# Performance work log

Hardware: AMD Instinct MI355X
Metric: run time of the kernel (lower is better)

## Reference

```python
import jax, jax.numpy as jnp
import numpy as np

SIZE = 48          # grid edge
DIST = 4           # local neighborhood edge
PAD = DIST // 2    # padding = 2
PADDED = SIZE + 2 * PAD  # 52
RATE = 5           # recurrent steps
CONVEY = 0.9
N_IN = 2048        # input injection sites


def setup_inputs() -> dict:
    key = jax.random.key(0)
    ks = jax.random.split(key, 8)
    neuron_matrix = jnp.zeros((PADDED, PADDED, PADDED), dtype=jnp.float32)
    vinput = jax.random.normal(ks[0], (N_IN,), dtype=jnp.float32)
    # scale synapse so the 5-step relu recurrence stays numerically tame
    synapse = jax.random.normal(ks[1], (SIZE, SIZE, SIZE, DIST, DIST, DIST), dtype=jnp.float32) * 0.05
    W1 = jax.random.normal(ks[2], (SIZE ** 3, 1024), dtype=jnp.float32) * (1.0 / np.sqrt(SIZE ** 3))
    b1 = jnp.zeros((1024,), dtype=jnp.float32)
    W2 = jax.random.normal(ks[3], (1024, 128), dtype=jnp.float32) * (1.0 / np.sqrt(1024))
    b2 = jnp.zeros((128,), dtype=jnp.float32)
    W3 = jax.random.normal(ks[4], (128, 10), dtype=jnp.float32) * (1.0 / np.sqrt(128))
    b3 = jnp.zeros((10,), dtype=jnp.float32)
    node_idx = jax.random.randint(ks[5], (N_IN, 3), 0, SIZE)  # interior coords
    return {"neuron_matrix": neuron_matrix, "vinput": vinput, "synapse": synapse,
            "W1": W1, "b1": b1, "W2": W2, "b2": b2, "W3": W3, "b3": b3,
            "node_idx": node_idx}


def _windows(p):
    # p: [PADDED]^3 -> sliding DxDxD windows at every interior site: [S,S,S,D,D,D]
    idx = jnp.arange(SIZE)[:, None] + jnp.arange(DIST)[None, :]  # [S, D]
    w = jnp.take(p, idx, axis=0)   # [S, D, P, P]
    w = jnp.take(w, idx, axis=2)   # [S, D, S, D, P]
    w = jnp.take(w, idx, axis=4)   # [S, D, S, D, S, D]
    return jnp.transpose(w, (0, 2, 4, 1, 3, 5))  # [S, S, S, D, D, D]


def reference(neuron_matrix, vinput, synapse, W1, b1, W2, b2, W3, b3, node_idx):
    # inject inputs at (possibly colliding) interior nodes (scatter-add, like +=)
    nm = neuron_matrix.at[node_idx[:, 0] + PAD,
                          node_idx[:, 1] + PAD,
                          node_idx[:, 2] + PAD].add(vinput)
    # recurrent locally-connected 3D neighbor aggregation, RATE steps
    for _ in range(RATE):
        win = _windows(nm)  # [S,S,S,D,D,D]
        agg = jnp.einsum('xyzabc,xyzabc->xyz', synapse, win)  # per-site unique-weight reduce
        interior = jax.nn.relu(agg) * CONVEY
        nm = jnp.pad(interior, PAD)  # re-pad with zeros for next step
    x = interior.reshape(1, SIZE ** 3)
    x = jax.nn.relu(x @ W1 + b1)
    x = jax.nn.relu(x @ W2 + b2)
    return x @ W3 + b3  # [1, 10]
```

## Files before the change

kernel.cpp:

```cpp
#include <hip/hip_runtime.h>

#define S 48
#define D 4
#define PADC 2
#define P 52
#define SITES (S * S * S)
#define PADVOL (P * P * P)
#define N_IN 2048
#define H1 1024
#define H2 128
#define OUTN 10
#define RP 64
#define NCH (SITES / RP)
#define RG 16
#define CHPG (NCH / RG)
#define G2B 32

__global__ __launch_bounds__(256) void zero_k(float4* __restrict__ p, int n4) {
    int i = blockIdx.x * 256 + threadIdx.x;
    if (i < n4) p[i] = make_float4(0.f, 0.f, 0.f, 0.f);
}

__global__ void scatter_k(const float* __restrict__ vin,
                          const int* __restrict__ idx,
                          float* __restrict__ nm) {
    int t = blockIdx.x * blockDim.x + threadIdx.x;
    if (t < N_IN) {
        int x = idx[t * 3 + 0] + PADC;
        int y = idx[t * 3 + 1] + PADC;
        int z = idx[t * 3 + 2] + PADC;
        atomicAdd(&nm[(x * P + y) * P + z], vin[t]);
    }
}

__global__ __launch_bounds__(256) void step_k(const float* __restrict__ src,
                                              const float* __restrict__ syn,
                                              float* __restrict__ dst) {
    int tid = threadIdx.x;
    int q = tid & 3;
    int sl = tid >> 2;
    int s = blockIdx.x * 64 + sl;
    int z = s % S;
    int t2 = s / S;
    int y = t2 % S;
    int x = t2 / S;
    const float4* sv = (const float4*)(syn + (size_t)s * 64);
    float acc = 0.0f;
#pragma unroll
    for (int a = 0; a < D; a++) {
        const float* row = src + ((x + a) * P + (y + q)) * P + z;
        float4 w = sv[a * 4 + q];
        acc += w.x * row[0] + w.y * row[1] + w.z * row[2] + w.w * row[3];
    }
    acc += __shfl_xor(acc, 1);
    acc += __shfl_xor(acc, 2);
    if (q == 0) {
        dst[((x + PADC) * P + (y + PADC)) * P + (z + PADC)] = fmaxf(acc, 0.0f) * 0.9f;
    }
}

__global__ __launch_bounds__(256) void gemv1_k(const float* __restrict__ nmfin,
                                               const float* __restrict__ W1,
                                               float* __restrict__ partial) {
    __shared__ float xs[RP];
    int t = threadIdx.x;
    int lane = t & 63;
    int i0 = blockIdx.x * RP;

    int i = i0 + lane;
    int z = i % S;
    int q = i / S;
    int y = q % S;
    int x = q / S;
    float v = nmfin[((x + PADC) * P + (y + PADC)) * P + (z + PADC)];
    unsigned long long mask = __ballot(v != 0.0f);
    if (t < RP) xs[t] = v;
    __syncthreads();

    const float4* W4 = (const float4*)W1;
    size_t base = (size_t)i0 * (H1 / 4) + t;
    float4 a0 = {0.f, 0.f, 0.f, 0.f};
    float4 a1 = {0.f, 0.f, 0.f, 0.f};
    while (mask) {
        int r0 = (int)__builtin_ctzll(mask);
        mask &= mask - 1;
        if (mask) {
            int r1 = (int)__builtin_ctzll(mask);
            mask &= mask - 1;
            float x0 = xs[r0], x1 = xs[r1];
            float4 w0 = W4[base + (size_t)r0 * (H1 / 4)];
            float4 w1 = W4[base + (size_t)r1 * (H1 / 4)];
            a0.x += x0 * w0.x; a0.y += x0 * w0.y; a0.z += x0 * w0.z; a0.w += x0 * w0.w;
            a1.x += x1 * w1.x; a1.y += x1 * w1.y; a1.z += x1 * w1.z; a1.w += x1 * w1.w;
        } else {
            float x0 = xs[r0];
            float4 w0 = W4[base + (size_t)r0 * (H1 / 4)];
            a0.x += x0 * w0.x; a0.y += x0 * w0.y; a0.z += x0 * w0.z; a0.w += x0 * w0.w;
        }
    }
    float4 acc = {a0.x + a1.x, a0.y + a1.y, a0.z + a1.z, a0.w + a1.w};
    ((float4*)(partial + (size_t)blockIdx.x * H1))[t] = acc;
}

__global__ __launch_bounds__(256) void reduceA_k(const float* __restrict__ partial,
                                                 float* __restrict__ redB) {
    int g = blockIdx.x >> 2;
    int c = (blockIdx.x & 3) * 256 + threadIdx.x;
    float s = 0.0f;
    int r0 = g * CHPG;
#pragma unroll 4
    for (int r = r0; r < r0 + CHPG; r++) s += partial[(size_t)r * H1 + c];
    redB[g * H1 + c] = s;
}

__global__ __launch_bounds__(128) void gemv2_k(const float* __restrict__ redB,
                                               const float* __restrict__ b1,
                                               const float* __restrict__ W2,
                                               float* __restrict__ partial2) {
    __shared__ float ys[H1 / G2B];
    int b = blockIdx.x;
    int t = threadIdx.x;
    int r0 = b * (H1 / G2B);
    if (t < H1 / G2B) {
        int j = r0 + t;
        float s = b1[j];
#pragma unroll
        for (int g = 0; g < RG; g++) s += redB[g * H1 + j];
        ys[t] = fmaxf(s, 0.0f);
    }
    __syncthreads();
    float acc = 0.0f;
#pragma unroll
    for (int i = 0; i < H1 / G2B; i++)
        acc += ys[i] * W2[(size_t)(r0 + i) * H2 + t];
    partial2[b * H2 + t] = acc;
}

__global__ __launch_bounds__(128) void final_k(const float* __restrict__ partial2,
                                               const float* __restrict__ b2,
                                               const float* __restrict__ W3,
                                               const float* __restrict__ b3,
                                               float* __restrict__ out) {
    __shared__ float y2[H2];
    int t = threadIdx.x;
    float s = b2[t];
#pragma unroll
    for (int k = 0; k < G2B; k++) s += partial2[k * H2 + t];
    y2[t] = fmaxf(s, 0.0f);
    __syncthreads();
    if (t < OUTN) {
        float o = b3[t];
#pragma unroll 8
        for (int i = 0; i < H2; i++) o += y2[i] * W3[i * OUTN + t];
        out[t] = o;
    }
}

extern "C" void kernel_launch(void* const* d_in, const int* in_sizes, int n_in,
                              void* d_out, int out_size, void* d_ws, size_t ws_size,
                              hipStream_t stream) {
    const float* vinput  = (const float*)d_in[1];
    const float* synapse = (const float*)d_in[2];
    const float* W1      = (const float*)d_in[3];
    const float* b1      = (const float*)d_in[4];
    const float* W2      = (const float*)d_in[5];
    const float* b2      = (const float*)d_in[6];
    const float* W3      = (const float*)d_in[7];
    const float* b3      = (const float*)d_in[8];
    const int* node_idx  = (const int*)d_in[9];

    float* ws = (float*)d_ws;
    float* nm0 = ws;
    float* nm1 = nm0 + PADVOL;
    float* partial1 = nm1 + PADVOL;
    float* redB = partial1 + (size_t)NCH * H1;
    float* partial2 = redB + RG * H1;
    float* out = (float*)d_out;

    const int n4 = 2 * PADVOL / 4;
    zero_k<<<(n4 + 255) / 256, 256, 0, stream>>>((float4*)nm0, n4);

    scatter_k<<<N_IN / 256, 256, 0, stream>>>(vinput, node_idx, nm0);

    const float* src = nm0;
    float* dst = nm1;
    for (int r = 0; r < 5; r++) {
        step_k<<<SITES / 64, 256, 0, stream>>>(src, synapse, dst);
        float* tmp = (float*)src;
        src = dst;
        dst = tmp;
    }

    gemv1_k<<<NCH, 256, 0, stream>>>(src, W1, partial1);
    reduceA_k<<<RG * 4, 256, 0, stream>>>(partial1, redB);
    gemv2_k<<<G2B, 128, 0, stream>>>(redB, b1, W2, partial2);
    final_k<<<1, 128, 0, stream>>>(partial2, b2, W3, b3, out);
}
```

Baseline: 93.50 us.

## Widen step threads per site, use readlane in gemv1, fold reduction into gemv2

The stencil step now assigns 8 threads per site, each handling two (a,b) rows, instead of 4 threads per site, which doubles the grid and adds one shuffle level. gemv1 broadcasts activations with readlane instead of shared memory plus a barrier, and unrolls the sparse loop by 4 for more loads in flight. The separate reduceA kernel is removed and gemv2 sums all partial rows itself, which saves a launch but leaves only 32 blocks to perform a long strided reduction.

```diff
diff --git a/kernel.cpp b/kernel.cpp
--- a/kernel.cpp
+++ b/kernel.cpp
@@ -12,8 +12,6 @@
 #define OUTN 10
 #define RP 64
 #define NCH (SITES / RP)
-#define RG 16
-#define CHPG (NCH / RG)
 #define G2B 32
 
 __global__ __launch_bounds__(256) void zero_k(float4* __restrict__ p, int n4) {
@@ -37,24 +35,28 @@
                                               const float* __restrict__ syn,
                                               float* __restrict__ dst) {
     int tid = threadIdx.x;
-    int q = tid & 3;
-    int sl = tid >> 2;
-    int s = blockIdx.x * 64 + sl;
+    int oct = tid & 7;
+    int sl = tid >> 3;
+    int s = blockIdx.x * 32 + sl;
     int z = s % S;
     int t2 = s / S;
     int y = t2 % S;
     int x = t2 / S;
+    int a = oct >> 1;
+    int b0 = (oct & 1) * 2;
     const float4* sv = (const float4*)(syn + (size_t)s * 64);
     float acc = 0.0f;
 #pragma unroll
-    for (int a = 0; a < D; a++) {
-        const float* row = src + ((x + a) * P + (y + q)) * P + z;
-        float4 w = sv[a * 4 + q];
+    for (int bb = 0; bb < 2; bb++) {
+        int b = b0 + bb;
+        const float* row = src + ((x + a) * P + (y + b)) * P + z;
+        float4 w = sv[a * 4 + b];
         acc += w.x * row[0] + w.y * row[1] + w.z * row[2] + w.w * row[3];
     }
     acc += __shfl_xor(acc, 1);
     acc += __shfl_xor(acc, 2);
-    if (q == 0) {
+    acc += __shfl_xor(acc, 4);
+    if (oct == 0) {
         dst[((x + PADC) * P + (y + PADC)) * P + (z + PADC)] = fmaxf(acc, 0.0f) * 0.9f;
     }
 }
@@ -62,7 +64,6 @@
 __global__ __launch_bounds__(256) void gemv1_k(const float* __restrict__ nmfin,
                                                const float* __restrict__ W1,
                                                float* __restrict__ partial) {
-    __shared__ float xs[RP];
     int t = threadIdx.x;
     int lane = t & 63;
     int i0 = blockIdx.x * RP;
@@ -74,65 +75,70 @@
     int x = q / S;
     float v = nmfin[((x + PADC) * P + (y + PADC)) * P + (z + PADC)];
     unsigned long long mask = __ballot(v != 0.0f);
-    if (t < RP) xs[t] = v;
-    __syncthreads();
 
     const float4* W4 = (const float4*)W1;
     size_t base = (size_t)i0 * (H1 / 4) + t;
     float4 a0 = {0.f, 0.f, 0.f, 0.f};
     float4 a1 = {0.f, 0.f, 0.f, 0.f};
+    float4 a2 = {0.f, 0.f, 0.f, 0.f};
+    float4 a3 = {0.f, 0.f, 0.f, 0.f};
+    int nnz = __popcll(mask);
+    for (int k = 0; k + 4 <= nnz; k += 4) {
+        int r0 = (int)__builtin_ctzll(mask); mask &= mask - 1;
+        int r1 = (int)__builtin_ctzll(mask); mask &= mask - 1;
+        int r2 = (int)__builtin_ctzll(mask); mask &= mask - 1;
+        int r3 = (int)__builtin_ctzll(mask); mask &= mask - 1;
+        float x0 = __int_as_float(__builtin_amdgcn_readlane(__float_as_int(v), r0));
+        float x1 = __int_as_float(__builtin_amdgcn_readlane(__float_as_int(v), r1));
+        float x2 = __int_as_float(__builtin_amdgcn_readlane(__float_as_int(v), r2));
+        float x3 = __int_as_float(__builtin_amdgcn_readlane(__float_as_int(v), r3));
+        float4 w0 = W4[base + (size_t)r0 * (H1 / 4)];
+        float4 w1 = W4[base + (size_t)r1 * (H1 / 4)];
+        float4 w2 = W4[base + (size_t)r2 * (H1 / 4)];
+        float4 w3 = W4[base + (size_t)r3 * (H1 / 4)];
+        a0.x += x0 * w0.x; a0.y += x0 * w0.y; a0.z += x0 * w0.z; a0.w += x0 * w0.w;
+        a1.x += x1 * w1.x; a1.y += x1 * w1.y; a1.z += x1 * w1.z; a1.w += x1 * w1.w;
+        a2.x += x2 * w2.x; a2.y += x2 * w2.y; a2.z += x2 * w2.z; a2.w += x2 * w2.w;
+        a3.x += x3 * w3.x; a3.y += x3 * w3.y; a3.z += x3 * w3.z; a3.w += x3 * w3.w;
+    }
     while (mask) {
-        int r0 = (int)__builtin_ctzll(mask);
-        mask &= mask - 1;
-        if (mask) {
-            int r1 = (int)__builtin_ctzll(mask);
-            mask &= mask - 1;
-            float x0 = xs[r0], x1 = xs[r1];
-            float4 w0 = W4[base + (size_t)r0 * (H1 / 4)];
-            float4 w1 = W4[base + (size_t)r1 * (H1 / 4)];
-            a0.x += x0 * w0.x; a0.y += x0 * w0.y; a0.z += x0 * w0.z; a0.w += x0 * w0.w;
-            a1.x += x1 * w1.x; a1.y += x1 * w1.y; a1.z += x1 * w1.z; a1.w += x1 * w1.w;
-        } else {
-            float x0 = xs[r0];
-            float4 w0 = W4[base + (size_t)r0 * (H1 / 4)];
-            a0.x += x0 * w0.x; a0.y += x0 * w0.y; a0.z += x0 * w0.z; a0.w += x0 * w0.w;
-        }
-    }
-    float4 acc = {a0.x + a1.x, a0.y + a1.y, a0.z + a1.z, a0.w + a1.w};
+        int r0 = (int)__builtin_ctzll(mask); mask &= mask - 1;
+        float x0 = __int_as_float(__builtin_amdgcn_readlane(__float_as_int(v), r0));
+        float4 w0 = W4[base + (size_t)r0 * (H1 / 4)];
+        a0.x += x0 * w0.x; a0.y += x0 * w0.y; a0.z += x0 * w0.z; a0.w += x0 * w0.w;
+    }
+    float4 acc = {a0.x + a1.x + a2.x + a3.x,
+                  a0.y + a1.y + a2.y + a3.y,
+                  a0.z + a1.z + a2.z + a3.z,
+                  a0.w + a1.w + a2.w + a3.w};
     ((float4*)(partial + (size_t)blockIdx.x * H1))[t] = acc;
 }
 
-__global__ __launch_bounds__(256) void reduceA_k(const float* __restrict__ partial,
-                                                 float* __restrict__ redB) {
-    int g = blockIdx.x >> 2;
-    int c = (blockIdx.x & 3) * 256 + threadIdx.x;
-    float s = 0.0f;
-    int r0 = g * CHPG;
-#pragma unroll 4
-    for (int r = r0; r < r0 + CHPG; r++) s += partial[(size_t)r * H1 + c];
-    redB[g * H1 + c] = s;
-}
-
-__global__ __launch_bounds__(128) void gemv2_k(const float* __restrict__ redB,
+__global__ __launch_bounds__(128) void gemv2_k(const float* __restrict__ partial1,
                                                const float* __restrict__ b1,
                                                const float* __restrict__ W2,
                                                float* __restrict__ partial2) {
-    __shared__ float ys[H1 / G2B];
+    __shared__ float ps[4][32];
+    __shared__ float ys[32];
+    int t = threadIdx.x;
     int b = blockIdx.x;
-    int t = threadIdx.x;
-    int r0 = b * (H1 / G2B);
-    if (t < H1 / G2B) {
-        int j = r0 + t;
-        float s = b1[j];
-#pragma unroll
-        for (int g = 0; g < RG; g++) s += redB[g * H1 + j];
-        ys[t] = fmaxf(s, 0.0f);
+    int r0 = b * 32;
+    int i = t & 31, g = t >> 5;
+    float s = 0.0f;
+#pragma unroll 8
+    for (int r = g; r < NCH; r += 4)
+        s += partial1[(size_t)r * H1 + r0 + i];
+    ps[g][i] = s;
+    __syncthreads();
+    if (t < 32) {
+        float sum = b1[r0 + t] + ps[0][t] + ps[1][t] + ps[2][t] + ps[3][t];
+        ys[t] = fmaxf(sum, 0.0f);
     }
     __syncthreads();
     float acc = 0.0f;
 #pragma unroll
-    for (int i = 0; i < H1 / G2B; i++)
-        acc += ys[i] * W2[(size_t)(r0 + i) * H2 + t];
+    for (int k = 0; k < 32; k++)
+        acc += ys[k] * W2[(size_t)(r0 + k) * H2 + t];
     partial2[b * H2 + t] = acc;
 }
 
@@ -173,8 +179,7 @@
     float* nm0 = ws;
     float* nm1 = nm0 + PADVOL;
     float* partial1 = nm1 + PADVOL;
-    float* redB = partial1 + (size_t)NCH * H1;
-    float* partial2 = redB + RG * H1;
+    float* partial2 = partial1 + (size_t)NCH * H1;
     float* out = (float*)d_out;
 
     const int n4 = 2 * PADVOL / 4;
@@ -185,14 +190,13 @@
     const float* src = nm0;
     float* dst = nm1;
     for (int r = 0; r < 5; r++) {
-        step_k<<<SITES / 64, 256, 0, stream>>>(src, synapse, dst);
+        step_k<<<SITES / 32, 256, 0, stream>>>(src, synapse, dst);
         float* tmp = (float*)src;
         src = dst;
         dst = tmp;
     }
 
     gemv1_k<<<NCH, 256, 0, stream>>>(src, W1, partial1);
-    reduceA_k<<<RG * 4, 256, 0, stream>>>(partial1, redB);
-    gemv2_k<<<G2B, 128, 0, stream>>>(redB, b1, W2, partial2);
+    gemv2_k<<<G2B, 128, 0, stream>>>(partial1, b1, W2, partial2);
     final_k<<<1, 128, 0, stream>>>(partial2, b2, W3, b3, out);
 }
```

New measurement: 103.4 us. 1.11x slower.
